# Optimization experiments

Hardware: AMD Instinct MI355X
Metric: run time of the kernel (lower is better)

The kernel has to match this reference:

```python
import jax, jax.numpy as jnp
import numpy as np

EPS = 1e-5


def conv2d(x, w, b=None, stride=1, padding=0, dilation=1, groups=1):
    out = jax.lax.conv_general_dilated(
        x, w, (stride, stride), [(padding, padding), (padding, padding)],
        rhs_dilation=(dilation, dilation),
        dimension_numbers=('NCHW', 'OIHW', 'NCHW'),
        feature_group_count=groups)
    if b is not None:
        out = out + b[None, :, None, None]
    return out


def unfold3(x):
    # torch nn.Unfold(kernel=3, padding=1), kept as [b, c, 9, h, w]
    # (channel-major ordering c*9+k, k = row-major kernel index, matches torch)
    b, c, h, w = x.shape
    xp = jnp.pad(x, ((0, 0), (0, 0), (1, 1), (1, 1)))
    return jnp.stack([xp[:, :, i:i + h, j:j + w]
                      for i in range(3) for j in range(3)], axis=2)


def setup_inputs():
    B, C, O, H, W = 8, 64, 64, 128, 128
    key = jax.random.key(0)
    ks = jax.random.split(key, 16)
    s = 0.05
    rn = lambda k, shape: jax.random.normal(k, shape, jnp.float32) * s
    return {
        'x': jax.random.normal(ks[0], (B, C, H, W), jnp.float32),
        'cdcm_conv1_w': rn(ks[1], (C, C, 1, 1)),
        'cdcm_conv1_b': jnp.zeros((C,), jnp.float32),
        'cdcm_w5': rn(ks[2], (C, C, 3, 3)),
        'cdcm_w7': rn(ks[3], (C, C, 3, 3)),
        'cdcm_w9': rn(ks[4], (C, C, 3, 3)),
        'cdcm_w11': rn(ks[5], (C, C, 3, 3)),
        'dsc_dw_w': rn(ks[6], (C, 1, 3, 3)),
        'dsc_dw_b': jnp.zeros((C,), jnp.float32),
        'dsc_pw_w': rn(ks[7], (C, C, 1, 1)),
        'dsc_pw_b': jnp.zeros((C,), jnp.float32),
        'gw_w': rn(ks[8], (C, 9, 9)),
        'gw_b': jnp.zeros((C, 9), jnp.float32),
        'gw_bn_g': jnp.ones((C, 9), jnp.float32),
        'gw_bn_b': jnp.zeros((C, 9), jnp.float32),
        'gw_bn_m': jnp.zeros((C, 9), jnp.float32),
        'gw_bn_v': jnp.ones((C, 9), jnp.float32),
        'conv_w': rn(ks[9], (O, C, 3, 3)),
        'conv_b': jnp.zeros((O,), jnp.float32),
        'fr_w': rn(ks[10], (O, O, 1, 1)),
        'fr_b': jnp.zeros((O,), jnp.float32),
        'ens_w': rn(ks[11], (3, O, O, 3, 3)),
        'ens_b': jnp.zeros((3, O), jnp.float32),
        'bn_g': jnp.ones((O,), jnp.float32),
        'bn_b': jnp.zeros((O,), jnp.float32),
        'bn_m': jnp.zeros((O,), jnp.float32),
        'bn_v': jnp.ones((O,), jnp.float32),
    }


def reference(x, cdcm_conv1_w, cdcm_conv1_b, cdcm_w5, cdcm_w7, cdcm_w9, cdcm_w11,
              dsc_dw_w, dsc_dw_b, dsc_pw_w, dsc_pw_b,
              gw_w, gw_b, gw_bn_g, gw_bn_b, gw_bn_m, gw_bn_v,
              conv_w, conv_b, fr_w, fr_b, ens_w, ens_b,
              bn_g, bn_b, bn_m, bn_v):
    C = x.shape[1]
    # ---- CDCM: relu -> 1x1 conv -> 4 dilated 3x3 convs, each through the
    # SAME DepthwiseSeparableConv instance, then summed ----
    y = conv2d(jax.nn.relu(x), cdcm_conv1_w, cdcm_conv1_b)

    def dsc(z):
        z = conv2d(z, dsc_dw_w, dsc_dw_b, padding=1, groups=C)
        return conv2d(z, dsc_pw_w, dsc_pw_b)

    y = sum(dsc(conv2d(y, w, padding=d, dilation=d))
            for w, d in ((cdcm_w5, 5), (cdcm_w7, 7), (cdcm_w9, 9), (cdcm_w11, 11)))

    b, c, h, w = y.shape
    patches = unfold3(y)  # [b, c, 9, h, w]

    # ---- dynamic weight generation: grouped 1x1 conv (groups=c, 9->9 per
    # group) + inference BatchNorm over the c*9 channels + softmax over the 9
    # patch positions ----
    gw = jnp.einsum('coi,bcihw->bcohw', gw_w, patches) + gw_b[None, :, :, None, None]
    scale = (gw_bn_g / jnp.sqrt(gw_bn_v + EPS))[None, :, :, None, None]
    gw = (gw - gw_bn_m[None, :, :, None, None]) * scale + gw_bn_b[None, :, :, None, None]
    wsm = jax.nn.softmax(gw, axis=2)

    # ---- involution core: the rearrange to (3h,3w) + stride-3 3x3 conv is
    # exactly a contraction of (patches * weights) with the conv kernel over
    # the 9 kernel positions (row-major kernel index == patch index) ----
    prod = patches * wsm  # [b, c, 9, h, w]
    O = conv_w.shape[0]
    out = jnp.einsum('bckhw,ock->bohw', prod, conv_w.reshape(O, c, 9)) + conv_b[None, :, None, None]

    # ---- feature reuse: conv1x1(conv_out) + conv_out ----
    out = conv2d(out, fr_w, fr_b) + out

    # ---- ensemble: mean of 3 conv3x3 ----
    out = jnp.mean(jnp.stack([conv2d(out, ens_w[i], ens_b[i], padding=1)
                              for i in range(3)]), axis=0)

    # ---- final BN (inference) + ReLU ----
    out = (out - bn_m[None, :, None, None]) * (bn_g / jnp.sqrt(bn_v + EPS))[None, :, None, None] \
          + bn_b[None, :, None, None]
    return jax.nn.relu(out)
```

## Files before the change

kernel.cpp:

```cpp
#include <hip/hip_runtime.h>
#include <hip/hip_bf16.h>
#include <hip/hip_fp16.h>

#define EPSV 1e-5f
#define Bn 8
#define Cn 64
#define Hn 128
#define Wn 128
#define Pn (Hn*Wn)
#define PR 150
#define PE 130
#define YPAD_ELEMS (Bn*PR*PR*Cn)

typedef _Float16 v8h __attribute__((ext_vector_type(8)));
typedef float v16f __attribute__((ext_vector_type(16)));
typedef unsigned short ushort8v __attribute__((ext_vector_type(8)));
typedef unsigned short ushort4v __attribute__((ext_vector_type(4)));

__device__ __forceinline__ unsigned short f2h(float v) {
  _Float16 h = (_Float16)v;
  return *reinterpret_cast<const unsigned short*>(&h);
}
__device__ __forceinline__ float h2f(unsigned short u) {
  return (float)(*reinterpret_cast<const _Float16*>(&u));
}

__device__ __forceinline__ v8h exp8h(v8h x) {
  union { v8h v; __half2 h[4]; } u; u.v = x;
  #pragma unroll
  for (int i = 0; i < 4; i++) u.h[i] = h2exp(u.h[i]);
  return u.v;
}
__device__ __forceinline__ v8h rcp8h(v8h x) {
  union { v8h v; __half2 h[4]; } u; u.v = x;
  #pragma unroll
  for (int i = 0; i < 4; i++) u.h[i] = h2rcp(u.h[i]);
  return u.v;
}

__device__ __forceinline__ void gload_lds16(const void* g, void* l) {
  __builtin_amdgcn_global_load_lds(
      (const __attribute__((address_space(1))) unsigned int*)g,
      (__attribute__((address_space(3))) unsigned int*)l, 16, 0, 0);
}

__device__ __forceinline__ size_t clb(int b, int row, int kb, int col, int PD) {
  return ((((size_t)b * PD + row) * 4 + kb) * PD + col) * 16;
}

__device__ __forceinline__ void swz_bh(int& b, int& h) {
  int bid = blockIdx.x;
  int w = (bid & 7) * 128 + (bid >> 3);
  b = w >> 7; h = w & 127;
}

__global__ __launch_bounds__(256) void k_prep(
    const float* __restrict__ w1, const float* __restrict__ w5,
    const float* __restrict__ w7, const float* __restrict__ w9,
    const float* __restrict__ w11, const float* __restrict__ pww,
    const float* __restrict__ frw, const float* __restrict__ cw,
    const float* __restrict__ gww, const float* __restrict__ gwb,
    const float* __restrict__ gbg, const float* __restrict__ gbb,
    const float* __restrict__ gbm, const float* __restrict__ gbv,
    const float* __restrict__ ensw, const float* __restrict__ ensb,
    const float* __restrict__ bng, const float* __restrict__ bnb,
    const float* __restrict__ bnm, const float* __restrict__ bnv,
    unsigned short* __restrict__ apack, unsigned short* __restrict__ apinv,
    unsigned short* __restrict__ apens, unsigned short* __restrict__ appw1,
    unsigned short* __restrict__ appw, unsigned short* __restrict__ apfr,
    unsigned short* __restrict__ gwpk,
    unsigned short* __restrict__ apk, unsigned short* __restrict__ bpk,
    float* __restrict__ esc, float* __restrict__ ebi,
    unsigned short* __restrict__ ypad, unsigned short* __restrict__ spad)
{
  int id = blockIdx.x * 256 + threadIdx.x;
  if (id < 147456) {
    int c0 = id / 9216;
    int d = c0 >> 2, kb = c0 & 3;
    int r = id - c0 * 9216;
    int t9 = r / 1024;
    int r2 = r & 1023;
    int mh = r2 >> 9, l = (r2 >> 3) & 63, e = r2 & 7;
    int m = mh * 32 + (l & 31);
    int c = kb * 16 + (l >> 5) * 8 + e;
    const float* src = (d == 0) ? w5 : (d == 1) ? w7 : (d == 2) ? w9 : w11;
    apack[id] = f2h(src[(m * 64 + c) * 9 + t9]);
    return;
  }
  id -= 147456;
  if (id < 36864) {
    int e = id & 7, l = (id >> 3) & 63, mh = (id >> 9) & 1,
        kb = (id >> 10) & 3, tap = id >> 12;
    int m = mh * 32 + (l & 31);
    int c = kb * 16 + (l >> 5) * 8 + e;
    apinv[id] = f2h(cw[(m * 64 + c) * 9 + tap]);
    return;
  }
  id -= 36864;
  if (id < 36864) {
    int e = id & 7, l = (id >> 3) & 63, mh = (id >> 9) & 1,
        kb = (id >> 10) & 3, tap = id >> 12;
    int m = mh * 32 + (l & 31);
    int c = kb * 16 + (l >> 5) * 8 + e;
    float v = (ensw[((0 * 64 + m) * 64 + c) * 9 + tap] +
               ensw[((64 + m) * 64 + c) * 9 + tap] +
               ensw[((128 + m) * 64 + c) * 9 + tap]) * (1.f / 3.f);
    apens[id] = f2h(v);
    return;
  }
  id -= 36864;
  if (id < 4096) {
    int e = id & 7, l = (id >> 3) & 63, mh = (id >> 9) & 1, kb = (id >> 10) & 3;
    int m = mh * 32 + (l & 31);
    int c = kb * 16 + (l >> 5) * 8 + e;
    appw1[id] = f2h(w1[m * 64 + c]);
    return;
  }
  id -= 4096;
  if (id < 4096) {
    int e = id & 7, l = (id >> 3) & 63, mh = (id >> 9) & 1, kb = (id >> 10) & 3;
    int m = mh * 32 + (l & 31);
    int c = kb * 16 + (l >> 5) * 8 + e;
    appw[id] = f2h(pww[m * 64 + c]);
    return;
  }
  id -= 4096;
  if (id < 4096) {
    int e = id & 7, l = (id >> 3) & 63, mh = (id >> 9) & 1, kb = (id >> 10) & 3;
    int m = mh * 32 + (l & 31);
    int c = kb * 16 + (l >> 5) * 8 + e;
    apfr[id] = f2h(frw[m * 64 + c]);
    return;
  }
  id -= 4096;
  if (id < 5184) {
    int cblk = id / 648, r = id - cblk * 648;
    int tap = r >> 3, ch = r & 7;
    int c = cblk * 8 + ch;
    gwpk[id] = f2h(gww[c * 81 + tap]);
    return;
  }
  id -= 5184;
  if (id < 576) {
    int cblk = id / 72, r = id - cblk * 72;
    int o = r >> 3, ch = r & 7;
    int c = cblk * 8 + ch;
    float A = gbg[c * 9 + o] / sqrtf(gbv[c * 9 + o] + EPSV);
    apk[id] = f2h(A);
    return;
  }
  id -= 576;
  if (id < 576) {
    int cblk = id / 72, r = id - cblk * 72;
    int o = r >> 3, ch = r & 7;
    int c = cblk * 8 + ch;
    float A = gbg[c * 9 + o] / sqrtf(gbv[c * 9 + o] + EPSV);
    float B = (gwb[c * 9 + o] - gbm[c * 9 + o]) * A + gbb[c * 9 + o];
    bpk[id] = f2h(B);
    return;
  }
  id -= 576;
  if (id < 64) {
    float s = bng[id] / sqrtf(bnv[id] + EPSV);
    esc[id] = s;
    float bm = (ensb[id] + ensb[64 + id] + ensb[128 + id]) * (1.f / 3.f);
    ebi[id] = (bm - bnm[id]) * s + bnb[id];
    return;
  }
  id -= 64;
  ushort8v z = {0, 0, 0, 0, 0, 0, 0, 0};
  const int perY = 22 * PR + 128 * 22;
  if (id < perY * Bn) {
    int b = id / perY; int r = id - b * perY;
    int tb = 22 * PR;
    int row, col;
    if (r < tb) {
      int rr = r / PR; col = r - rr * PR;
      row = (rr < 11) ? rr : (rr + 128);
    } else {
      int r2 = r - tb;
      row = 11 + r2 / 22;
      int cc = r2 % 22;
      col = (cc < 11) ? cc : (cc + 128);
    }
    #pragma unroll
    for (int kb = 0; kb < 4; kb++) {
      unsigned short* p = ypad + clb(b, row, kb, col, PR);
      *(ushort8v*)p = z;
      *(ushort8v*)(p + 8) = z;
    }
    return;
  }
  id -= perY * Bn;
  const int perS = 2 * PE + 256;
  if (id < perS * Bn) {
    int b = id / perS; int r = id - b * perS;
    int tb = 2 * PE;
    int row, col;
    if (r < tb) {
      int rr = r / PE; col = r - rr * PE;
      row = (rr < 1) ? 0 : 129;
    } else {
      int r2 = r - tb;
      row = 1 + r2 / 2;
      col = (r2 & 1) ? 129 : 0;
    }
    #pragma unroll
    for (int kb = 0; kb < 4; kb++) {
      unsigned short* p = spad + clb(b, row, kb, col, PE);
      *(ushort8v*)p = z;
      *(ushort8v*)(p + 8) = z;
    }
  }
}

__global__ __launch_bounds__(256, 4) void k_pw1x(const float* __restrict__ x,
    const unsigned short* __restrict__ apw, const float* __restrict__ bias,
    unsigned short* __restrict__ ypad)
{
  int b, h; swz_bh(b, h);
  const int tid = threadIdx.x, wv = tid >> 6, l = tid & 63;
  const int ln31 = l & 31, g = l >> 5;
  const int px = wv * 32 + ln31;
  const float* xb = x + ((size_t)b * Cn) * Pn + h * Wn + px;
  v16f acc0, acc1;
  #pragma unroll
  for (int r = 0; r < 16; r++) { acc0[r] = 0.f; acc1[r] = 0.f; }
  const unsigned short* apl = apw + l * 8;
  #pragma unroll
  for (int kb = 0; kb < 4; kb++) {
    int c0 = kb * 16 + g * 8;
    v8h Bf;
    #pragma unroll
    for (int e = 0; e < 8; e++)
      Bf[e] = (_Float16)fmaxf(xb[(size_t)(c0 + e) * Pn], 0.f);
    v8h A0 = *(const v8h*)(apl + (kb * 2) * 512);
    v8h A1 = *(const v8h*)(apl + (kb * 2 + 1) * 512);
    acc0 = __builtin_amdgcn_mfma_f32_32x32x16_f16(A0, Bf, acc0, 0, 0, 0);
    acc1 = __builtin_amdgcn_mfma_f32_32x32x16_f16(A1, Bf, acc1, 0, 0, 0);
  }
  #pragma unroll
  for (int t = 0; t < 4; t++) {
    int c0 = 8 * t + 4 * g;
    int kb = c0 >> 4, sub = c0 & 15;
    ushort4v s0, s1;
    #pragma unroll
    for (int u = 0; u < 4; u++) {
      s0[u] = f2h(acc0[4 * t + u] + bias[c0 + u]);
      s1[u] = f2h(acc1[4 * t + u] + bias[c0 + u + 32]);
    }
    *(ushort4v*)(ypad + clb(b, h + 11, kb, px + 11, PR) + sub) = s0;
    *(ushort4v*)(ypad + clb(b, h + 11, kb + 2, px + 11, PR) + sub) = s1;
  }
}

__global__ __launch_bounds__(1024, 1) void k_cdcm_mfma(
    const unsigned short* __restrict__ ypad,
    const unsigned short* __restrict__ apack,
    unsigned short* __restrict__ spad)
{
  __shared__ __align__(16) unsigned short Abuf[2][9216];
  const int bid = blockIdx.x;
  const int b = bid & 7, rg = bid >> 3;
  const int tid = threadIdx.x, wv = tid >> 6, l = tid & 63;
  const int ln31 = l & 31, g = l >> 5;
  const int h = rg * 4 + (wv >> 2);
  const int seg = (wv & 3) * 32;
  const int ng = (wv < 2) ? 2 : 1;

  {
    const char* src = (const char*)apack;
    char* dst = (char*)&Abuf[0][0];
    for (int i = 0; i < ng; i++) {
      int off = (wv + i * 16) * 1024;
      gload_lds16(src + off + l * 16, dst + off);
    }
  }

  v16f acc0, acc1;
  #pragma unroll
  for (int r = 0; r < 16; r++) { acc0[r] = 0.f; acc1[r] = 0.f; }

  #pragma unroll
  for (int d = 0; d < 4; d++) {
    const int dil = 5 + 2 * d;
    #pragma unroll
    for (int kb = 0; kb < 4; kb++) {
      const int ci = d * 4 + kb;
      if (ci < 15) {
        const char* src = (const char*)(apack + (ci + 1) * 9216);
        char* dst = (char*)&Abuf[(ci + 1) & 1][0];
        for (int i = 0; i < ng; i++) {
          int off = (wv + i * 16) * 1024;
          gload_lds16(src + off + l * 16, dst + off);
        }
        if (wv < 2) asm volatile("s_waitcnt vmcnt(2)" ::: "memory");
        else        asm volatile("s_waitcnt vmcnt(1)" ::: "memory");
      } else {
        asm volatile("s_waitcnt vmcnt(0)" ::: "memory");
      }
      asm volatile("s_barrier" ::: "memory");

      __builtin_amdgcn_s_setprio(1);
      const unsigned short* abl = &Abuf[ci & 1][0] + l * 8;
      #pragma unroll
      for (int ky = 0; ky < 3; ky++) {
        const int row = h + 11 + (ky - 1) * dil;
        #pragma unroll
        for (int kx = 0; kx < 3; kx++) {
          const int col = seg + ln31 + (kx - 1) * dil + 11;
          const int t9 = ky * 3 + kx;
          v8h Bf = *(const v8h*)(ypad + clb(b, row, kb, col, PR) + g * 8);
          const unsigned short* ap = abl + t9 * 1024;
          v8h A0 = *(const v8h*)(ap);
          v8h A1 = *(const v8h*)(ap + 512);
          acc0 = __builtin_amdgcn_mfma_f32_32x32x16_f16(A0, Bf, acc0, 0, 0, 0);
          acc1 = __builtin_amdgcn_mfma_f32_32x32x16_f16(A1, Bf, acc1, 0, 0, 0);
        }
      }
      __builtin_amdgcn_s_setprio(0);
      asm volatile("s_barrier" ::: "memory");
    }
  }
  const int px = seg + ln31;
  #pragma unroll
  for (int t = 0; t < 4; t++) {
    int c0 = 8 * t + 4 * g;
    int kb = c0 >> 4, sub = c0 & 15;
    ushort4v s0, s1;
    #pragma unroll
    for (int u = 0; u < 4; u++) {
      s0[u] = f2h(acc0[4 * t + u]);
      s1[u] = f2h(acc1[4 * t + u]);
    }
    *(ushort4v*)(spad + clb(b, h + 1, kb, px + 1, PE) + sub) = s0;
    *(ushort4v*)(spad + clb(b, h + 1, kb + 2, px + 1, PE) + sub) = s1;
  }
}

__global__ __launch_bounds__(256, 4) void k_dwpw_mfma(
    const unsigned short* __restrict__ spad,
    const float* __restrict__ dww, const float* __restrict__ dwb,
    const unsigned short* __restrict__ appw, const float* __restrict__ pwb,
    unsigned short* __restrict__ y2pad)
{
  __shared__ float wdw[576];
  __shared__ float bdw[64];
  const int tid = threadIdx.x;
  for (int t = tid; t < 576; t += 256) wdw[t] = dww[t];
  if (tid < 64) bdw[tid] = dwb[tid];
  __syncthreads();

  int b, h; swz_bh(b, h);

  ushort8v z = {0, 0, 0, 0, 0, 0, 0, 0};
  if (h == 0) {
    for (int px = tid; px < 260; px += 256) {
      int row = (px < 130) ? 0 : 129;
      int col = (px < 130) ? px : px - 130;
      #pragma unroll
      for (int kb = 0; kb < 4; kb++) {
        unsigned short* p = y2pad + clb(b, row, kb, col, PE);
        *(ushort8v*)p = z;
        *(ushort8v*)(p + 8) = z;
      }
    }
  } else if (h == 1) {
    int row = 1 + (tid & 127);
    int col = (tid >> 7) ? 129 : 0;
    #pragma unroll
    for (int kb = 0; kb < 4; kb++) {
      unsigned short* p = y2pad + clb(b, row, kb, col, PE);
      *(ushort8v*)p = z;
      *(ushort8v*)(p + 8) = z;
    }
  }

  const int wv = tid >> 6, l = tid & 63;
  const int ln31 = l & 31, g = l >> 5;
  const int w = wv * 32 + ln31;

  v16f acc0, acc1;
  #pragma unroll
  for (int r = 0; r < 16; r++) { acc0[r] = 0.f; acc1[r] = 0.f; }
  const unsigned short* apl = appw + l * 8;

  #pragma unroll
  for (int kb = 0; kb < 4; kb++) {
    const int c0 = kb * 16 + g * 8;
    v8h t[9];
    #pragma unroll
    for (int k = 0; k < 9; k++) {
      const int dy = k / 3 - 1, dx = k % 3 - 1;
      t[k] = *(const v8h*)(spad + clb(b, h + 1 + dy, kb, w + 1 + dx, PE) + g * 8);
    }
    v8h dvh;
    #pragma unroll
    for (int e = 0; e < 8; e++) {
      const int c = c0 + e;
      float a = 4.f * bdw[c];
      #pragma unroll
      for (int k = 0; k < 9; k++) a += wdw[c * 9 + k] * (float)t[k][e];
      dvh[e] = (_Float16)a;
    }
    v8h A0 = *(const v8h*)(apl + (kb * 2) * 512);
    v8h A1 = *(const v8h*)(apl + (kb * 2 + 1) * 512);
    acc0 = __builtin_amdgcn_mfma_f32_32x32x16_f16(A0, dvh, acc0, 0, 0, 0);
    acc1 = __builtin_amdgcn_mfma_f32_32x32x16_f16(A1, dvh, acc1, 0, 0, 0);
  }
  #pragma unroll
  for (int t = 0; t < 4; t++) {
    int c0 = 8 * t + 4 * g;
    int kb = c0 >> 4, sub = c0 & 15;
    ushort4v s0, s1;
    #pragma unroll
    for (int u = 0; u < 4; u++) {
      s0[u] = f2h(acc0[4 * t + u] + 4.f * pwb[c0 + u]);
      s1[u] = f2h(acc1[4 * t + u] + 4.f * pwb[c0 + u + 32]);
    }
    *(ushort4v*)(y2pad + clb(b, h + 1, kb, w + 1, PE) + sub) = s0;
    *(ushort4v*)(y2pad + clb(b, h + 1, kb + 2, w + 1, PE) + sub) = s1;
  }
}

__global__ __launch_bounds__(256, 3) void k_invol_mfma(
    const unsigned short* __restrict__ y2pad,
    const unsigned short* __restrict__ gwpk,
    const unsigned short* __restrict__ apk,
    const unsigned short* __restrict__ bpk,
    const unsigned short* __restrict__ apinv,
    const float* __restrict__ cbias,
    unsigned short* __restrict__ ipad)
{
  __shared__ __align__(16) unsigned short gws[5184];
  __shared__ __align__(16) unsigned short As[576];
  __shared__ __align__(16) unsigned short Bs[576];
  const int tid = threadIdx.x;
  for (int t = tid; t < 648; t += 256)
    ((ushort8v*)gws)[t] = ((const ushort8v*)gwpk)[t];
  if (tid < 72) {
    ((ushort8v*)As)[tid] = ((const ushort8v*)apk)[tid];
    ((ushort8v*)Bs)[tid] = ((const ushort8v*)bpk)[tid];
  }
  __syncthreads();

  int b, h; swz_bh(b, h);
  const int wv = tid >> 6, l = tid & 63;
  const int p32 = l & 31, g = l >> 5;
  const int w = wv * 32 + p32;

  v16f acc0, acc1;
  #pragma unroll
  for (int r = 0; r < 16; r++) { acc0[r] = 0.f; acc1[r] = 0.f; }

  for (int cb4 = 0; cb4 < 4; cb4++) {
    const int cblk = cb4 * 2 + g;
    const unsigned short* gwp = gws + cblk * 648;
    const unsigned short* Ap = As + cblk * 72;
    const unsigned short* Bp = Bs + cblk * 72;

    v8h pt[9];
    #pragma unroll
    for (int k = 0; k < 9; k++) {
      const int dy = k / 3 - 1, dx = k % 3 - 1;
      pt[k] = *(const v8h*)(y2pad + clb(b, h + 1 + dy, cb4, w + 1 + dx, PE) + g * 8);
    }
    v8h s[9];
    #pragma unroll
    for (int o = 0; o < 9; o++) {
      v8h a = (*(const v8h*)(gwp + o * 72)) * pt[0];
      #pragma unroll
      for (int i = 1; i < 9; i++)
        a += (*(const v8h*)(gwp + o * 72 + i * 8)) * pt[i];
      s[o] = a * (*(const v8h*)(Ap + o * 8)) + (*(const v8h*)(Bp + o * 8));
    }
    v8h esum = {0, 0, 0, 0, 0, 0, 0, 0};
    #pragma unroll
    for (int o = 0; o < 9; o++) { s[o] = exp8h(s[o]); esum += s[o]; }
    v8h inv = rcp8h(esum);
    #pragma unroll
    for (int k = 0; k < 9; k++) pt[k] = pt[k] * s[k] * inv;

    const unsigned short* ap = apinv + l * 8;
    __builtin_amdgcn_s_setprio(1);
    #pragma unroll
    for (int k = 0; k < 9; k++) {
      const unsigned short* a2 = ap + ((k * 4 + cb4) * 2) * 512;
      v8h A0 = *(const v8h*)(a2);
      v8h A1 = *(const v8h*)(a2 + 512);
      acc0 = __builtin_amdgcn_mfma_f32_32x32x16_f16(A0, pt[k], acc0, 0, 0, 0);
      acc1 = __builtin_amdgcn_mfma_f32_32x32x16_f16(A1, pt[k], acc1, 0, 0, 0);
    }
    __builtin_amdgcn_s_setprio(0);
  }
  #pragma unroll
  for (int t = 0; t < 4; t++) {
    int c0 = 8 * t + 4 * g;
    int kb = c0 >> 4, sub = c0 & 15;
    ushort4v s0, s1;
    #pragma unroll
    for (int u = 0; u < 4; u++) {
      s0[u] = f2h(acc0[4 * t + u] + cbias[c0 + u]);
      s1[u] = f2h(acc1[4 * t + u] + cbias[c0 + u + 32]);
    }
    *(ushort4v*)(ipad + clb(b, h, kb, w, 128) + sub) = s0;
    *(ushort4v*)(ipad + clb(b, h, kb + 2, w, 128) + sub) = s1;
  }
}

__global__ __launch_bounds__(256, 4) void k_fr_mfma(
    const unsigned short* __restrict__ ipad,
    const unsigned short* __restrict__ apfr,
    const float* __restrict__ bias,
    unsigned short* __restrict__ opad)
{
  int b, h; swz_bh(b, h);
  const int tid = threadIdx.x, wv = tid >> 6, l = tid & 63;
  const int ln31 = l & 31, g = l >> 5;
  const int px = wv * 32 + ln31;
  v16f acc0, acc1;
  #pragma unroll
  for (int r = 0; r < 16; r++) { acc0[r] = 0.f; acc1[r] = 0.f; }
  const unsigned short* apl = apfr + l * 8;
  #pragma unroll
  for (int kb = 0; kb < 4; kb++) {
    v8h Bf = *(const v8h*)(ipad + clb(b, h, kb, px, 128) + g * 8);
    v8h A0 = *(const v8h*)(apl + (kb * 2) * 512);
    v8h A1 = *(const v8h*)(apl + (kb * 2 + 1) * 512);
    acc0 = __builtin_amdgcn_mfma_f32_32x32x16_f16(A0, Bf, acc0, 0, 0, 0);
    acc1 = __builtin_amdgcn_mfma_f32_32x32x16_f16(A1, Bf, acc1, 0, 0, 0);
  }
  #pragma unroll
  for (int t = 0; t < 4; t++) {
    int c0 = 8 * t + 4 * g;
    int kb = c0 >> 4, sub = c0 & 15;
    ushort4v r0 = *(const ushort4v*)(ipad + clb(b, h, kb, px, 128) + sub);
    ushort4v r1 = *(const ushort4v*)(ipad + clb(b, h, kb + 2, px, 128) + sub);
    ushort4v s0, s1;
    #pragma unroll
    for (int u = 0; u < 4; u++) {
      s0[u] = f2h(acc0[4 * t + u] + bias[c0 + u] + h2f(r0[u]));
      s1[u] = f2h(acc1[4 * t + u] + bias[c0 + u + 32] + h2f(r1[u]));
    }
    *(ushort4v*)(opad + clb(b, h + 1, kb, px + 1, PE) + sub) = s0;
    *(ushort4v*)(opad + clb(b, h + 1, kb + 2, px + 1, PE) + sub) = s1;
  }
}

__global__ __launch_bounds__(256) void k_ens_mfma(
    const unsigned short* __restrict__ opad,
    const unsigned short* __restrict__ apens,
    const float* __restrict__ esc, const float* __restrict__ ebi,
    float* __restrict__ out)
{
  __shared__ __align__(16) unsigned short Abuf[36864];
  const int tid = threadIdx.x;
  {
    const ushort8v* src = (const ushort8v*)apens;
    ushort8v* dst = (ushort8v*)Abuf;
    #pragma unroll
    for (int it = 0; it < 18; it++)
      dst[tid + it * 256] = src[tid + it * 256];
  }
  __syncthreads();

  const int bid = blockIdx.x;
  const int b = bid & 7, h0 = (bid >> 3) * 2;
  const int wv = tid >> 6, l = tid & 63;
  const int ln31 = l & 31, g = l >> 5;

  v16f a00, a01, a10, a11;
  #pragma unroll
  for (int r = 0; r < 16; r++) { a00[r] = 0.f; a01[r] = 0.f; a10[r] = 0.f; a11[r] = 0.f; }

  const unsigned short* abl = Abuf + l * 8;

  #pragma unroll
  for (int ky = 0; ky < 3; ky++) {
    #pragma unroll
    for (int kx = 0; kx < 3; kx++) {
      const int tap = ky * 3 + kx;
      const int r0 = h0 + ky;
      const int col = wv * 32 + ln31 + kx;
      const unsigned short* ap = abl + tap * 4096;
      #pragma unroll
      for (int kb = 0; kb < 4; kb++) {
        v8h B0 = *(const v8h*)(opad + clb(b, r0, kb, col, PE) + g * 8);
        v8h B1 = *(const v8h*)(opad + clb(b, r0 + 1, kb, col, PE) + g * 8);
        v8h A0 = *(const v8h*)(ap + kb * 1024);
        v8h A1 = *(const v8h*)(ap + kb * 1024 + 512);
        a00 = __builtin_amdgcn_mfma_f32_32x32x16_f16(A0, B0, a00, 0, 0, 0);
        a01 = __builtin_amdgcn_mfma_f32_32x32x16_f16(A1, B0, a01, 0, 0, 0);
        a10 = __builtin_amdgcn_mfma_f32_32x32x16_f16(A0, B1, a10, 0, 0, 0);
        a11 = __builtin_amdgcn_mfma_f32_32x32x16_f16(A1, B1, a11, 0, 0, 0);
      }
    }
  }
  float* sp0 = out + ((size_t)b * Cn) * Pn + h0 * Wn + wv * 32 + ln31;
  float* sp1 = sp0 + Wn;
  #pragma unroll
  for (int r = 0; r < 16; r++) {
    int o0 = (r & 3) + 8 * (r >> 2) + 4 * g;
    float e0 = esc[o0], e1 = esc[o0 + 32];
    float i0 = ebi[o0], i1 = ebi[o0 + 32];
    sp0[(size_t)o0 * Pn] = fmaxf(a00[r] * e0 + i0, 0.f);
    sp0[(size_t)(o0 + 32) * Pn] = fmaxf(a01[r] * e1 + i1, 0.f);
    sp1[(size_t)o0 * Pn] = fmaxf(a10[r] * e0 + i0, 0.f);
    sp1[(size_t)(o0 + 32) * Pn] = fmaxf(a11[r] * e1 + i1, 0.f);
  }
}

extern "C" void kernel_launch(void* const* d_in, const int* in_sizes, int n_in,
                              void* d_out, int out_size, void* d_ws, size_t ws_size,
                              hipStream_t stream)
{
  const float* x    = (const float*)d_in[0];
  const float* w1   = (const float*)d_in[1];
  const float* b1   = (const float*)d_in[2];
  const float* w5   = (const float*)d_in[3];
  const float* w7   = (const float*)d_in[4];
  const float* w9   = (const float*)d_in[5];
  const float* w11  = (const float*)d_in[6];
  const float* dww  = (const float*)d_in[7];
  const float* dwb  = (const float*)d_in[8];
  const float* pww  = (const float*)d_in[9];
  const float* pwb  = (const float*)d_in[10];
  const float* gww  = (const float*)d_in[11];
  const float* gwb  = (const float*)d_in[12];
  const float* gbg  = (const float*)d_in[13];
  const float* gbb  = (const float*)d_in[14];
  const float* gbm  = (const float*)d_in[15];
  const float* gbv  = (const float*)d_in[16];
  const float* cw   = (const float*)d_in[17];
  const float* cb   = (const float*)d_in[18];
  const float* frw  = (const float*)d_in[19];
  const float* frb  = (const float*)d_in[20];
  const float* ensw = (const float*)d_in[21];
  const float* ensb = (const float*)d_in[22];
  const float* bng  = (const float*)d_in[23];
  const float* bnb  = (const float*)d_in[24];
  const float* bnm  = (const float*)d_in[25];
  const float* bnv  = (const float*)d_in[26];

  unsigned short* wsu   = (unsigned short*)d_ws;
  unsigned short* ypad  = wsu;
  unsigned short* y2pad = wsu;
  unsigned short* opad  = wsu;
  unsigned short* apack = wsu + YPAD_ELEMS;
  unsigned short* apinv = apack + 147456;
  unsigned short* apens = apinv + 36864;
  unsigned short* appw1 = apens + 36864;
  unsigned short* appw  = appw1 + 4096;
  unsigned short* apfr  = appw + 4096;
  unsigned short* gwpk  = apfr + 4096;
  unsigned short* apk   = gwpk + 5184;
  unsigned short* bpk   = apk + 576;
  float* esc = (float*)(bpk + 576);
  float* ebi = esc + 64;

  unsigned short* spad = (unsigned short*)d_out;
  unsigned short* ipad = (unsigned short*)d_out;
  float* D = (float*)d_out;

  k_prep<<<1145, 256, 0, stream>>>(w1, w5, w7, w9, w11, pww, frw, cw,
                                   gww, gwb, gbg, gbb, gbm, gbv, ensw, ensb,
                                   bng, bnb, bnm, bnv,
                                   apack, apinv, apens, appw1, appw, apfr,
                                   gwpk, apk, bpk, esc, ebi,
                                   ypad, spad);

  k_pw1x<<<1024, 256, 0, stream>>>(x, appw1, b1, ypad);
  k_cdcm_mfma<<<256, 1024, 0, stream>>>(ypad, apack, spad);
  k_dwpw_mfma<<<1024, 256, 0, stream>>>(spad, dww, dwb, appw, pwb, y2pad);
  k_invol_mfma<<<1024, 256, 0, stream>>>(y2pad, gwpk, apk, bpk, apinv, cb, ipad);
  k_fr_mfma<<<1024, 256, 0, stream>>>(ipad, apfr, frb, opad);
  k_ens_mfma<<<512, 256, 0, stream>>>(opad, apens, esc, ebi, D);
}
```

Before: 146.3 us.

## Double-buffer two channel blocks per stage in cdcm and vectorize depthwise in fp16

The dilated-conv kernel now stages two channel blocks of packed weights into LDS per pipeline step, which halves the number of barrier/waitcnt rounds at the cost of twice the LDS footprint. The depthwise conv in the dw+pw kernel now uses fp16 packed weights prepared in the prep kernel, computing with vector half FMAs instead of per-element fp32 loops reading weights from LDS. It also removes that kernel's LDS staging and __syncthreads. The fp16 accumulation over 9 taps reduces precision.

```diff
diff --git a/kernel.cpp b/kernel.cpp
--- a/kernel.cpp
+++ b/kernel.cpp
@@ -65,11 +65,13 @@
     const float* __restrict__ ensw, const float* __restrict__ ensb,
     const float* __restrict__ bng, const float* __restrict__ bnb,
     const float* __restrict__ bnm, const float* __restrict__ bnv,
+    const float* __restrict__ dww, const float* __restrict__ dwb,
     unsigned short* __restrict__ apack, unsigned short* __restrict__ apinv,
     unsigned short* __restrict__ apens, unsigned short* __restrict__ appw1,
     unsigned short* __restrict__ appw, unsigned short* __restrict__ apfr,
     unsigned short* __restrict__ gwpk,
     unsigned short* __restrict__ apk, unsigned short* __restrict__ bpk,
+    unsigned short* __restrict__ dwpk, unsigned short* __restrict__ bdwpk,
     float* __restrict__ esc, float* __restrict__ ebi,
     unsigned short* __restrict__ ypad, unsigned short* __restrict__ spad)
 {
@@ -160,6 +162,19 @@
     return;
   }
   id -= 576;
+  if (id < 576) {
+    int cblk = id / 72, r = id - cblk * 72;
+    int tap = r >> 3, ch = r & 7;
+    int c = cblk * 8 + ch;
+    dwpk[id] = f2h(dww[c * 9 + tap]);
+    return;
+  }
+  id -= 576;
+  if (id < 64) {
+    bdwpk[id] = f2h(4.f * dwb[id]);
+    return;
+  }
+  id -= 64;
   if (id < 64) {
     float s = bng[id] / sqrtf(bnv[id] + EPSV);
     esc[id] = s;
@@ -259,14 +274,14 @@
     const unsigned short* __restrict__ apack,
     unsigned short* __restrict__ spad)
 {
-  __shared__ __align__(16) unsigned short Abuf[2][9216];
+  __shared__ __align__(16) unsigned short Abuf[2][18432];
   const int bid = blockIdx.x;
   const int b = bid & 7, rg = bid >> 3;
   const int tid = threadIdx.x, wv = tid >> 6, l = tid & 63;
   const int ln31 = l & 31, g = l >> 5;
   const int h = rg * 4 + (wv >> 2);
   const int seg = (wv & 3) * 32;
-  const int ng = (wv < 2) ? 2 : 1;
+  const int ng = (wv < 4) ? 3 : 2;
 
   {
     const char* src = (const char*)apack;
@@ -282,27 +297,28 @@
   for (int r = 0; r < 16; r++) { acc0[r] = 0.f; acc1[r] = 0.f; }
 
   #pragma unroll
-  for (int d = 0; d < 4; d++) {
+  for (int pp = 0; pp < 8; pp++) {
+    const int d = pp >> 1, kbp = pp & 1;
     const int dil = 5 + 2 * d;
-    #pragma unroll
-    for (int kb = 0; kb < 4; kb++) {
-      const int ci = d * 4 + kb;
-      if (ci < 15) {
-        const char* src = (const char*)(apack + (ci + 1) * 9216);
-        char* dst = (char*)&Abuf[(ci + 1) & 1][0];
-        for (int i = 0; i < ng; i++) {
-          int off = (wv + i * 16) * 1024;
-          gload_lds16(src + off + l * 16, dst + off);
-        }
-        if (wv < 2) asm volatile("s_waitcnt vmcnt(2)" ::: "memory");
-        else        asm volatile("s_waitcnt vmcnt(1)" ::: "memory");
-      } else {
-        asm volatile("s_waitcnt vmcnt(0)" ::: "memory");
+    if (pp < 7) {
+      const char* src = (const char*)(apack + (pp + 1) * 18432);
+      char* dst = (char*)&Abuf[(pp + 1) & 1][0];
+      for (int i = 0; i < ng; i++) {
+        int off = (wv + i * 16) * 1024;
+        gload_lds16(src + off + l * 16, dst + off);
       }
-      asm volatile("s_barrier" ::: "memory");
-
-      __builtin_amdgcn_s_setprio(1);
-      const unsigned short* abl = &Abuf[ci & 1][0] + l * 8;
+      if (wv < 4) asm volatile("s_waitcnt vmcnt(3)" ::: "memory");
+      else        asm volatile("s_waitcnt vmcnt(2)" ::: "memory");
+    } else {
+      asm volatile("s_waitcnt vmcnt(0)" ::: "memory");
+    }
+    asm volatile("s_barrier" ::: "memory");
+
+    __builtin_amdgcn_s_setprio(1);
+    const unsigned short* abl = &Abuf[pp & 1][0] + l * 8;
+    #pragma unroll
+    for (int kbl = 0; kbl < 2; kbl++) {
+      const int kb = kbp * 2 + kbl;
       #pragma unroll
       for (int ky = 0; ky < 3; ky++) {
         const int row = h + 11 + (ky - 1) * dil;
@@ -311,16 +327,16 @@
           const int col = seg + ln31 + (kx - 1) * dil + 11;
           const int t9 = ky * 3 + kx;
           v8h Bf = *(const v8h*)(ypad + clb(b, row, kb, col, PR) + g * 8);
-          const unsigned short* ap = abl + t9 * 1024;
+          const unsigned short* ap = abl + kbl * 9216 + t9 * 1024;
           v8h A0 = *(const v8h*)(ap);
           v8h A1 = *(const v8h*)(ap + 512);
           acc0 = __builtin_amdgcn_mfma_f32_32x32x16_f16(A0, Bf, acc0, 0, 0, 0);
           acc1 = __builtin_amdgcn_mfma_f32_32x32x16_f16(A1, Bf, acc1, 0, 0, 0);
         }
       }
-      __builtin_amdgcn_s_setprio(0);
-      asm volatile("s_barrier" ::: "memory");
-    }
+    }
+    __builtin_amdgcn_s_setprio(0);
+    asm volatile("s_barrier" ::: "memory");
   }
   const int px = seg + ln31;
   #pragma unroll
@@ -340,17 +356,12 @@
 
 __global__ __launch_bounds__(256, 4) void k_dwpw_mfma(
     const unsigned short* __restrict__ spad,
-    const float* __restrict__ dww, const float* __restrict__ dwb,
+    const unsigned short* __restrict__ dwpk,
+    const unsigned short* __restrict__ bdwpk,
     const unsigned short* __restrict__ appw, const float* __restrict__ pwb,
     unsigned short* __restrict__ y2pad)
 {
-  __shared__ float wdw[576];
-  __shared__ float bdw[64];
   const int tid = threadIdx.x;
-  for (int t = tid; t < 576; t += 256) wdw[t] = dww[t];
-  if (tid < 64) bdw[tid] = dwb[tid];
-  __syncthreads();
-
   int b, h; swz_bh(b, h);
 
   ushort8v z = {0, 0, 0, 0, 0, 0, 0, 0};
@@ -387,26 +398,22 @@
 
   #pragma unroll
   for (int kb = 0; kb < 4; kb++) {
-    const int c0 = kb * 16 + g * 8;
+    const int cblk = kb * 2 + g;
+    const unsigned short* wp = dwpk + cblk * 72;
     v8h t[9];
     #pragma unroll
     for (int k = 0; k < 9; k++) {
       const int dy = k / 3 - 1, dx = k % 3 - 1;
       t[k] = *(const v8h*)(spad + clb(b, h + 1 + dy, kb, w + 1 + dx, PE) + g * 8);
     }
-    v8h dvh;
-    #pragma unroll
-    for (int e = 0; e < 8; e++) {
-      const int c = c0 + e;
-      float a = 4.f * bdw[c];
-      #pragma unroll
-      for (int k = 0; k < 9; k++) a += wdw[c * 9 + k] * (float)t[k][e];
-      dvh[e] = (_Float16)a;
-    }
+    v8h dv = *(const v8h*)(bdwpk + cblk * 8);
+    #pragma unroll
+    for (int k = 0; k < 9; k++)
+      dv += (*(const v8h*)(wp + k * 8)) * t[k];
     v8h A0 = *(const v8h*)(apl + (kb * 2) * 512);
     v8h A1 = *(const v8h*)(apl + (kb * 2 + 1) * 512);
-    acc0 = __builtin_amdgcn_mfma_f32_32x32x16_f16(A0, dvh, acc0, 0, 0, 0);
-    acc1 = __builtin_amdgcn_mfma_f32_32x32x16_f16(A1, dvh, acc1, 0, 0, 0);
+    acc0 = __builtin_amdgcn_mfma_f32_32x32x16_f16(A0, dv, acc0, 0, 0, 0);
+    acc1 = __builtin_amdgcn_mfma_f32_32x32x16_f16(A1, dv, acc1, 0, 0, 0);
   }
   #pragma unroll
   for (int t = 0; t < 4; t++) {
@@ -655,23 +662,25 @@
   unsigned short* gwpk  = apfr + 4096;
   unsigned short* apk   = gwpk + 5184;
   unsigned short* bpk   = apk + 576;
-  float* esc = (float*)(bpk + 576);
+  unsigned short* dwpk  = bpk + 576;
+  unsigned short* bdwpk = dwpk + 576;
+  float* esc = (float*)(bdwpk + 64);
   float* ebi = esc + 64;
 
   unsigned short* spad = (unsigned short*)d_out;
   unsigned short* ipad = (unsigned short*)d_out;
   float* D = (float*)d_out;
 
-  k_prep<<<1145, 256, 0, stream>>>(w1, w5, w7, w9, w11, pww, frw, cw,
+  k_prep<<<1147, 256, 0, stream>>>(w1, w5, w7, w9, w11, pww, frw, cw,
                                    gww, gwb, gbg, gbb, gbm, gbv, ensw, ensb,
-                                   bng, bnb, bnm, bnv,
+                                   bng, bnb, bnm, bnv, dww, dwb,
                                    apack, apinv, apens, appw1, appw, apfr,
-                                   gwpk, apk, bpk, esc, ebi,
+                                   gwpk, apk, bpk, dwpk, bdwpk, esc, ebi,
                                    ypad, spad);
 
   k_pw1x<<<1024, 256, 0, stream>>>(x, appw1, b1, ypad);
   k_cdcm_mfma<<<256, 1024, 0, stream>>>(ypad, apack, spad);
-  k_dwpw_mfma<<<1024, 256, 0, stream>>>(spad, dww, dwb, appw, pwb, y2pad);
+  k_dwpw_mfma<<<1024, 256, 0, stream>>>(spad, dwpk, bdwpk, appw, pwb, y2pad);
   k_invol_mfma<<<1024, 256, 0, stream>>>(y2pad, gwpk, apk, bpk, apinv, cb, ipad);
   k_fr_mfma<<<1024, 256, 0, stream>>>(ipad, apfr, frb, opad);
   k_ens_mfma<<<512, 256, 0, stream>>>(opad, apens, esc, ebi, D);
```

New measurement: 154.3 us. +5.5%, slower.
